# Optimization experiments

Hardware: AMD Instinct MI355X
Metric: run time of the kernel (lower is better)

The kernel has to match this reference:

```python
import jax, jax.numpy as jnp
import numpy as np

N = 100_000      # nodes
E = 1_600_000    # edges (avg degree 16)
D_IN, D_H, D_OUT = 128, 128, 64


def setup_inputs() -> dict:
    key = jax.random.key(0)
    ks = jax.random.split(key, 6)
    x = jax.random.normal(ks[0], (N, D_IN), jnp.float32)
    edge_index = jax.random.randint(ks[1], (2, E), 0, N, dtype=jnp.int32)
    W1 = jax.random.normal(ks[2], (D_IN, D_H), jnp.float32) / np.sqrt(D_IN)
    b1 = jnp.zeros((D_H,), jnp.float32)
    W2 = jax.random.normal(ks[3], (D_H, D_OUT), jnp.float32) / np.sqrt(D_H)
    b2 = jnp.zeros((D_OUT,), jnp.float32)
    return {"x": x, "edge_index": edge_index, "W1": W1, "b1": b1, "W2": W2, "b2": b2}


def _gcn_layer(x, W, b, src, dst, n_nodes):
    # PyG GCNConv: h = x @ W; symmetric norm with self-loops; scatter-add; + bias
    h = x @ W                                        # [N, D_out]
    deg = jax.ops.segment_sum(jnp.ones_like(dst, jnp.float32), dst,
                              num_segments=n_nodes)  # self-loops => deg >= 1
    dinv = jax.lax.rsqrt(deg)                        # deg^{-1/2}
    norm = dinv[src] * dinv[dst]                     # [E+N]
    msg = h[src] * norm[:, None]                     # gather + scale
    out = jax.ops.segment_sum(msg, dst, num_segments=n_nodes)  # scatter-add
    return out + b


def reference(x, edge_index, W1, b1, W2, b2):
    n = x.shape[0]
    loop = jnp.arange(n, dtype=edge_index.dtype)
    src = jnp.concatenate([edge_index[0], loop])     # add self-loops
    dst = jnp.concatenate([edge_index[1], loop])
    h = _gcn_layer(x, W1, b1, src, dst, n)
    h = jax.nn.relu(h)
    # dropout(p=0.5) is identity in eval mode
    out = _gcn_layer(h, W2, b2, src, dst, n)
    return out
```

## Files before the change

### kernel.cpp

```cpp
#include <hip/hip_runtime.h>
#include <hip/hip_bf16.h>


#define NTHREADS 256
#define BSH 9
#define NBMAX 256

typedef unsigned int uint;
typedef unsigned short ushort;
typedef __attribute__((ext_vector_type(8))) short short8;
typedef __attribute__((ext_vector_type(4))) float floatx4;

__device__ __forceinline__ uint pack_bf16(float a, float b) {
    __hip_bfloat162 h = __float22bfloat162_rn(make_float2(a, b));
    return *reinterpret_cast<uint*>(&h);
}
__device__ __forceinline__ float bf16_lo(uint q) { return __uint_as_float(q << 16); }
__device__ __forceinline__ float bf16_hi(uint q) { return __uint_as_float(q & 0xffff0000u); }

__global__ __launch_bounds__(256) void bucket_hist_kernel(
    const int* __restrict__ dst, int* __restrict__ bcnt, int e, int nb) {
    __shared__ int hist[NBMAX];
    int t = threadIdx.x;
    for (int b = t; b < nb; b += 256) hist[b] = 0;
    __syncthreads();
    int e0 = blockIdx.x * 2048;
#pragma unroll
    for (int v = 0; v < 2; v++) {
        int gi = e0 + t * 8 + v * 4;
        if (gi + 3 < e) {
            int4 d4 = *(const int4*)&dst[gi];
            atomicAdd(&hist[d4.x >> BSH], 1);
            atomicAdd(&hist[d4.y >> BSH], 1);
            atomicAdd(&hist[d4.z >> BSH], 1);
            atomicAdd(&hist[d4.w >> BSH], 1);
        } else {
            for (int j = 0; j < 4; j++)
                if (gi + j < e) atomicAdd(&hist[dst[gi + j] >> BSH], 1);
        }
    }
    __syncthreads();
    for (int b = t; b < nb; b += 256) {
        int v = hist[b];
        if (v) atomicAdd(&bcnt[b], v);
    }
}

__global__ void bucket_scan(const int* __restrict__ bcnt, int* __restrict__ bstart,
                            int* __restrict__ bcursor, int nb) {
    __shared__ int buf[NBMAX];
    int t = threadIdx.x;
    int v = (t < nb) ? bcnt[t] : 0;
    buf[t] = v;
    __syncthreads();
    int x = v;
    for (int off = 1; off < NBMAX; off <<= 1) {
        int y = (t >= off) ? buf[t - off] : 0;
        __syncthreads();
        x += y;
        buf[t] = x;
        __syncthreads();
    }
    if (t < nb) {
        bstart[t] = x - v;
        bcursor[t] = x - v;
    }
}

__global__ __launch_bounds__(256) void partition_kernel(
    const int* __restrict__ src, const int* __restrict__ dst,
    int* __restrict__ bcursor, int2* __restrict__ staged, int e, int nb) {
    __shared__ int eS[2048];
    __shared__ int eD[2048];
    __shared__ int hist[NBMAX];
    __shared__ int base[NBMAX];
    int t = threadIdx.x;
    int e0 = blockIdx.x * 2048;

    for (int b = t; b < nb; b += 256) hist[b] = 0;
    __syncthreads();
#pragma unroll
    for (int v = 0; v < 2; v++) {
        int li = t * 8 + v * 4;
        int gi = e0 + li;
        int4 s4, d4;
        if (gi + 3 < e) {
            s4 = *(const int4*)&src[gi];
            d4 = *(const int4*)&dst[gi];
        } else {
            const int* sp = &src[gi];
            const int* dp = &dst[gi];
            s4.x = (gi + 0 < e) ? sp[0] : 0;  d4.x = (gi + 0 < e) ? dp[0] : -1;
            s4.y = (gi + 1 < e) ? sp[1] : 0;  d4.y = (gi + 1 < e) ? dp[1] : -1;
            s4.z = (gi + 2 < e) ? sp[2] : 0;  d4.z = (gi + 2 < e) ? dp[2] : -1;
            s4.w = (gi + 3 < e) ? sp[3] : 0;  d4.w = (gi + 3 < e) ? dp[3] : -1;
        }
        *(int4*)&eS[li] = s4;
        *(int4*)&eD[li] = d4;
        if (d4.x >= 0) atomicAdd(&hist[d4.x >> BSH], 1);
        if (d4.y >= 0) atomicAdd(&hist[d4.y >> BSH], 1);
        if (d4.z >= 0) atomicAdd(&hist[d4.z >> BSH], 1);
        if (d4.w >= 0) atomicAdd(&hist[d4.w >> BSH], 1);
    }
    __syncthreads();
    for (int b = t; b < nb; b += 256) {
        int v = hist[b];
        base[b] = v ? atomicAdd(&bcursor[b], v) : 0;
        hist[b] = 0;
    }
    __syncthreads();
#pragma unroll
    for (int i = 0; i < 8; i++) {
        int li = t + i * 256;
        int d = eD[li];
        if (d >= 0) {
            int b = d >> BSH;
            int r = atomicAdd(&hist[b], 1);
            staged[base[b] + r] = make_int2(eS[li], d);
        }
    }
}

__global__ __launch_bounds__(256) void fine_csr_kernel(
    const int2* __restrict__ staged, const int* __restrict__ bstart,
    const int* __restrict__ bcnt, int4* __restrict__ meta,
    float* __restrict__ dinv, int* __restrict__ rec, int n) {
    __shared__ int lcnt[512];
    __shared__ int tsum[256];
    int b = blockIdx.x;
    int t = threadIdx.x;
    lcnt[t] = 0;
    lcnt[t + 256] = 0;
    __syncthreads();
    int s0 = bstart[b];
    int m = bcnt[b];
    for (int i = t; i < m; i += 256)
        atomicAdd(&lcnt[staged[s0 + i].y & 511], 1);
    __syncthreads();
    int v0 = lcnt[2 * t];
    int v1 = lcnt[2 * t + 1];
    int tot = v0 + v1;
    tsum[t] = tot;
    __syncthreads();
    int x = tot;
    for (int off = 1; off < 256; off <<= 1) {
        int y = (t >= off) ? tsum[t - off] : 0;
        __syncthreads();
        x += y;
        tsum[t] = x;
        __syncthreads();
    }
    int excl = x - tot;
    int node = (b << BSH) + 2 * t;
    if (node < n) {
        float di = rsqrtf((float)v0 + 1.0f);
        dinv[node] = di;
        meta[node] = make_int4(s0 + excl, v0, __float_as_int(di), __float_as_int(di * di));
    }
    if (node + 1 < n) {
        float di = rsqrtf((float)v1 + 1.0f);
        dinv[node + 1] = di;
        meta[node + 1] = make_int4(s0 + excl + v0, v1, __float_as_int(di), __float_as_int(di * di));
    }
    lcnt[2 * t] = s0 + excl;
    lcnt[2 * t + 1] = s0 + excl + v0;
    __syncthreads();
    for (int i = t; i < m; i += 256) {
        int2 ed = staged[s0 + i];
        int li = ed.y & 511;
        int pos = atomicAdd(&lcnt[li], 1);
        rec[pos] = ed.x;
    }
}

template <int COLS, bool XF32>
__global__ __launch_bounds__(256) void gemm_mfma(const void* __restrict__ Xv,
                                                 const float* __restrict__ W,
                                                 uint* __restrict__ Cq, int n) {
    __shared__ ushort sX[64 * 128];
    __shared__ ushort sWT[COLS * 128];
    int t = threadIdx.x;
    int rbase = blockIdx.x * 64;

    if (XF32) {
        const float* X = (const float*)Xv;
#pragma unroll
        for (int i = 0; i < 8; i++) {
            int f = t + 256 * i;
            int r = f >> 5;
            int c4 = f & 31;
            float4 v = make_float4(0.f, 0.f, 0.f, 0.f);
            int gr = rbase + r;
            if (gr < n) v = *(const float4*)(X + (size_t)gr * 128 + c4 * 4);
            uint lo = pack_bf16(v.x, v.y);
            uint hi = pack_bf16(v.z, v.w);
            int chunk = c4 >> 1;
            int sub = (c4 & 1) * 4;
            int off = r * 128 + (((chunk ^ (r & 15)) << 3) + sub);
            *(uint2*)&sX[off] = make_uint2(lo, hi);
        }
    } else {
        const ushort* X = (const ushort*)Xv;
#pragma unroll
        for (int i = 0; i < 4; i++) {
            int f = t + 256 * i;
            int r = f >> 4;
            int chunk = f & 15;
            uint4 v = make_uint4(0, 0, 0, 0);
            int gr = rbase + r;
            if (gr < n) v = *(const uint4*)(X + (size_t)gr * 128 + chunk * 8);
            int off = r * 128 + ((chunk ^ (r & 15)) << 3);
            *(uint4*)&sX[off] = v;
        }
    }
    {
        constexpr int UNITS = 64 * (COLS / 4);
        constexpr int PER_T = UNITS / 256;
#pragma unroll
        for (int i = 0; i < PER_T; i++) {
            int u = t + 256 * i;
            int kp = u / (COLS / 4);
            int n4 = u % (COLS / 4);
            int k = kp * 2;
            float4 w0 = *(const float4*)(W + (size_t)k * COLS + n4 * 4);
            float4 w1 = *(const float4*)(W + (size_t)(k + 1) * COLS + n4 * 4);
            int chunk = k >> 3;
            int sub = k & 7;
            const float* a0 = (const float*)&w0;
            const float* a1 = (const float*)&w1;
#pragma unroll
            for (int j = 0; j < 4; j++) {
                int nn = n4 * 4 + j;
                uint pk = pack_bf16(a0[j], a1[j]);
                int off = nn * 128 + (((chunk ^ (nn & 15)) << 3) + sub);
                *(uint*)&sWT[off] = pk;
            }
        }
    }
    __syncthreads();

    int lane = t & 63;
    int wave = t >> 6;
    int m = lane & 15;
    int q = lane >> 4;
    int r0 = wave * 16;

    floatx4 acc[COLS / 16];
#pragma unroll
    for (int c = 0; c < COLS / 16; c++) acc[c] = (floatx4){0.f, 0.f, 0.f, 0.f};

#pragma unroll
    for (int ks = 0; ks < 4; ks++) {
        int rr = r0 + m;
        int ca = (ks * 4 + q) ^ (rr & 15);
        short8 afrag = *(const short8*)&sX[rr * 128 + (ca << 3)];
#pragma unroll
        for (int c = 0; c < COLS / 16; c++) {
            int nn = c * 16 + m;
            int cb = (ks * 4 + q) ^ (nn & 15);
            short8 bfrag = *(const short8*)&sWT[nn * 128 + (cb << 3)];
            acc[c] = __builtin_amdgcn_mfma_f32_16x16x32_bf16(bfrag, afrag, acc[c], 0, 0, 0);
        }
    }

    int gr = rbase + r0 + m;
    if (gr < n) {
#pragma unroll
        for (int c = 0; c < COLS / 16; c++) {
            uint2 pk;
            pk.x = pack_bf16(acc[c][0], acc[c][1]);
            pk.y = pack_bf16(acc[c][2], acc[c][3]);
            *(uint2*)&Cq[(size_t)gr * (COLS / 2) + c * 8 + q * 2] = pk;
        }
    }
}

__global__ __launch_bounds__(512) void agg128_mm64(
    const uint* __restrict__ hq, const int* __restrict__ rec,
    const int4* __restrict__ meta, const float* __restrict__ dinv,
    const float* __restrict__ bias, const float* __restrict__ W2,
    uint* __restrict__ h2q, int n) {
    __shared__ ushort sWT[64 * 128];
    __shared__ ushort sg[16 * 128];
    int t = threadIdx.x;

#pragma unroll
    for (int i = 0; i < 2; i++) {
        int u = t + 512 * i;
        int kp = u >> 4;
        int n4 = u & 15;
        int k = kp * 2;
        float4 w0 = *(const float4*)(W2 + (size_t)k * 64 + n4 * 4);
        float4 w1 = *(const float4*)(W2 + (size_t)(k + 1) * 64 + n4 * 4);
        int chunk = k >> 3;
        int sub = k & 7;
        const float* a0f = (const float*)&w0;
        const float* a1f = (const float*)&w1;
#pragma unroll
        for (int j = 0; j < 4; j++) {
            int nn = n4 * 4 + j;
            uint pk = pack_bf16(a0f[j], a1f[j]);
            *(uint*)&sWT[nn * 128 + (((chunk ^ (nn & 15)) << 3) + sub)] = pk;
        }
    }

    int hw = t >> 5;
    int fl = t & 31;
    int nb0 = blockIdx.x * 16;
    int w = nb0 + hw;
    bool valid = w < n;
    int wsafe = valid ? w : 0;
    const uint2* h2 = (const uint2*)hq;

    int4 mt = meta[wsafe];
    int j0 = mt.x;
    int deg = valid ? mt.y : 0;
    float di = __int_as_float(mt.z);
    float swq = valid ? __int_as_float(mt.w) : 0.f;

    uint2 qs = h2[(size_t)wsafe * 32 + fl];
    float a0 = bf16_lo(qs.x) * swq, a1 = bf16_hi(qs.x) * swq;
    float a2 = bf16_lo(qs.y) * swq, a3 = bf16_hi(qs.y) * swq;

    const int* rp = rec + j0;
    int tt = 0;
    for (; tt + 8 <= deg; tt += 8) {
        uint2 q[8]; float wf[8];
#pragma unroll
        for (int u = 0; u < 8; u++) {
            int s = rp[tt + u];
            wf[u] = dinv[s] * di;
            q[u] = h2[(size_t)s * 32 + fl];
        }
#pragma unroll
        for (int u = 0; u < 8; u++) {
            a0 += bf16_lo(q[u].x) * wf[u]; a1 += bf16_hi(q[u].x) * wf[u];
            a2 += bf16_lo(q[u].y) * wf[u]; a3 += bf16_hi(q[u].y) * wf[u];
        }
    }
    for (; tt + 2 <= deg; tt += 2) {
        int s0i = rp[tt], s1i = rp[tt + 1];
        float w0v = dinv[s0i] * di, w1v = dinv[s1i] * di;
        uint2 q0 = h2[(size_t)s0i * 32 + fl];
        uint2 q1 = h2[(size_t)s1i * 32 + fl];
        a0 += bf16_lo(q0.x) * w0v + bf16_lo(q1.x) * w1v;
        a1 += bf16_hi(q0.x) * w0v + bf16_hi(q1.x) * w1v;
        a2 += bf16_lo(q0.y) * w0v + bf16_lo(q1.y) * w1v;
        a3 += bf16_hi(q0.y) * w0v + bf16_hi(q1.y) * w1v;
    }
    if (tt < deg) {
        int s = rp[tt];
        float wv = dinv[s] * di;
        uint2 q = h2[(size_t)s * 32 + fl];
        a0 += bf16_lo(q.x) * wv; a1 += bf16_hi(q.x) * wv;
        a2 += bf16_lo(q.y) * wv; a3 += bf16_hi(q.y) * wv;
    }

    float4 bb = *(const float4*)&bias[4 * fl];
    float o0 = fmaxf(a0 + bb.x, 0.f);
    float o1 = fmaxf(a1 + bb.y, 0.f);
    float o2 = fmaxf(a2 + bb.z, 0.f);
    float o3 = fmaxf(a3 + bb.w, 0.f);
    {
        int chunk = fl >> 1;
        int sub = (fl & 1) * 4;
        *(uint2*)&sg[hw * 128 + (((chunk ^ hw) << 3) + sub)] =
            make_uint2(pack_bf16(o0, o1), pack_bf16(o2, o3));
    }
    __syncthreads();

    int wave = t >> 6;
    int lane = t & 63;
    if (wave < 4) {
        int m = lane & 15;
        int q = lane >> 4;
        floatx4 acc = (floatx4){0.f, 0.f, 0.f, 0.f};
#pragma unroll
        for (int ks = 0; ks < 4; ks++) {
            int ca = (ks * 4 + q) ^ m;
            short8 afrag = *(const short8*)&sg[m * 128 + (ca << 3)];
            int nn = wave * 16 + m;
            int cb = (ks * 4 + q) ^ (nn & 15);
            short8 bfrag = *(const short8*)&sWT[nn * 128 + (cb << 3)];
            acc = __builtin_amdgcn_mfma_f32_16x16x32_bf16(bfrag, afrag, acc, 0, 0, 0);
        }
        int gr = nb0 + m;
        if (gr < n) {
            uint2 pk;
            pk.x = pack_bf16(acc[0], acc[1]);
            pk.y = pack_bf16(acc[2], acc[3]);
            *(uint2*)&h2q[(size_t)gr * 32 + wave * 8 + q * 2] = pk;
        }
    }
}

__global__ __launch_bounds__(256) void aggregate64q(
    const uint* __restrict__ hq, const int* __restrict__ rec,
    const int4* __restrict__ meta, const float* __restrict__ dinv,
    const float* __restrict__ bias, float* __restrict__ out, int n) {
    int w = (int)((blockIdx.x * blockDim.x + threadIdx.x) >> 5);
    if (w >= n) return;
    int fl = threadIdx.x & 31;

    int4 mt = meta[w];
    int j0 = mt.x;
    int deg = mt.y;
    float di = __int_as_float(mt.z);
    float swq = __int_as_float(mt.w);

    uint qs = hq[(size_t)w * 32 + fl];
    float a0 = bf16_lo(qs) * swq;
    float a1 = bf16_hi(qs) * swq;

    const int* rp = rec + j0;
    int t = 0;
    for (; t + 8 <= deg; t += 8) {
        uint q[8]; float wf[8];
#pragma unroll
        for (int u = 0; u < 8; u++) {
            int s = rp[t + u];
            wf[u] = dinv[s] * di;
            q[u] = hq[(size_t)s * 32 + fl];
        }
#pragma unroll
        for (int u = 0; u < 8; u++) {
            a0 += bf16_lo(q[u]) * wf[u];
            a1 += bf16_hi(q[u]) * wf[u];
        }
    }
    for (; t + 2 <= deg; t += 2) {
        int s0i = rp[t], s1i = rp[t + 1];
        float w0v = dinv[s0i] * di, w1v = dinv[s1i] * di;
        uint q0 = hq[(size_t)s0i * 32 + fl];
        uint q1 = hq[(size_t)s1i * 32 + fl];
        a0 += bf16_lo(q0) * w0v + bf16_lo(q1) * w1v;
        a1 += bf16_hi(q0) * w0v + bf16_hi(q1) * w1v;
    }
    if (t < deg) {
        int s = rp[t];
        float wv = dinv[s] * di;
        uint q = hq[(size_t)s * 32 + fl];
        a0 += bf16_lo(q) * wv;
        a1 += bf16_hi(q) * wv;
    }

    float2 bb = *(const float2*)&bias[2 * fl];
    float2 o;
    o.x = a0 + bb.x;
    o.y = a1 + bb.y;
    ((float2*)out)[(size_t)w * 32 + fl] = o;
}

extern "C" void kernel_launch(void* const* d_in, const int* in_sizes, int n_in,
                              void* d_out, int out_size, void* d_ws, size_t ws_size,
                              hipStream_t stream) {
    const float* x = (const float*)d_in[0];
    const int* edge = (const int*)d_in[1];
    const float* W1 = (const float*)d_in[2];
    const float* b1 = (const float*)d_in[3];
    const float* W2 = (const float*)d_in[4];
    const float* b2 = (const float*)d_in[5];

    const int N = in_sizes[0] / 128;
    const int E = in_sizes[1] / 2;
    const int* src = edge;
    const int* dst = edge + E;
    const int NB = (N + (1 << BSH) - 1) >> BSH;

    char* p = (char*)d_ws;
    int* bcnt = (int*)p;      p += NBMAX * 4;
    int* bstart = (int*)p;    p += NBMAX * 4;
    int* bcursor = (int*)p;   p += NBMAX * 4;
    float* dinv = (float*)p;  p += (size_t)N * 4;
    int4* meta = (int4*)p;    p += (size_t)N * 16;
    int* rec = (int*)p;       p += (size_t)E * 4;
    int2* staged = (int2*)p;  p += (size_t)E * 8;
    uint* hq = (uint*)p;      p += (size_t)N * 64 * 4;
    uint* h2q = (uint*)p;     p += (size_t)N * 32 * 4;

    float* out = (float*)d_out;
    const int eblocks = (E + 2047) / 2048;

    (void)hipMemsetAsync(bcnt, 0, NBMAX * 4, stream);
    bucket_hist_kernel<<<eblocks, 256, 0, stream>>>(dst, bcnt, E, NB);
    bucket_scan<<<1, NBMAX, 0, stream>>>(bcnt, bstart, bcursor, NB);
    partition_kernel<<<eblocks, 256, 0, stream>>>(src, dst, bcursor, staged, E, NB);
    fine_csr_kernel<<<NB, 256, 0, stream>>>(staged, bstart, bcnt, meta, dinv, rec, N);

    const int gblocks = (N + 63) / 64;

    gemm_mfma<128, true><<<gblocks, 256, 0, stream>>>(x, W1, hq, N);
    agg128_mm64<<<(N + 15) / 16, 512, 0, stream>>>(hq, rec, meta, dinv, b1, W2, h2q, N);
    aggregate64q<<<(N + 7) / 8, 256, 0, stream>>>(h2q, rec, meta, dinv, b2, out, N);
}
```

Measured before the change: 298.0 us.

## Fold source-side degree norm into GEMM epilogues and widen aggregation loads

Applies the source-side deg^-1/2 factor once per node in the GEMM and MM epilogues, so the aggregation loops no longer gather dinv per edge and only sum features before a final di scale. The aggregation kernels move from 32 lanes per node to 16 lanes per node (128-wide) and 8 lanes per node (64-wide) using 16-byte loads, and agg128_mm64 now handles 32 nodes per block with all 8 waves doing MFMA. This removes one dependent scattered load per edge and cuts instruction count, at the cost of rounding the pre-scaled values to bf16 and fewer lanes per node.

Measured after the change: 295.0 us. Within noise of the previous version (-1.0%).

```diff
diff --git a/kernel.cpp b/kernel.cpp
--- a/kernel.cpp
+++ b/kernel.cpp
@@ -176,7 +176,9 @@
 template <int COLS, bool XF32>
 __global__ __launch_bounds__(256) void gemm_mfma(const void* __restrict__ Xv,
                                                  const float* __restrict__ W,
-                                                 uint* __restrict__ Cq, int n) {
+                                                 uint* __restrict__ Cq,
+                                                 const float* __restrict__ dscale,
+                                                 int n) {
     __shared__ ushort sX[64 * 128];
     __shared__ ushort sWT[COLS * 128];
     int t = threadIdx.x;
@@ -265,11 +267,12 @@
 
     int gr = rbase + r0 + m;
     if (gr < n) {
+        float sc = dscale[gr];
 #pragma unroll
         for (int c = 0; c < COLS / 16; c++) {
             uint2 pk;
-            pk.x = pack_bf16(acc[c][0], acc[c][1]);
-            pk.y = pack_bf16(acc[c][2], acc[c][3]);
+            pk.x = pack_bf16(acc[c][0] * sc, acc[c][1] * sc);
+            pk.y = pack_bf16(acc[c][2] * sc, acc[c][3] * sc);
             *(uint2*)&Cq[(size_t)gr * (COLS / 2) + c * 8 + q * 2] = pk;
         }
     }
@@ -281,7 +284,7 @@
     const float* __restrict__ bias, const float* __restrict__ W2,
     uint* __restrict__ h2q, int n) {
     __shared__ ushort sWT[64 * 128];
-    __shared__ ushort sg[16 * 128];
+    __shared__ ushort sg[32 * 128];
     int t = threadIdx.x;
 
 #pragma unroll
@@ -304,151 +307,169 @@
         }
     }
 
-    int hw = t >> 5;
-    int fl = t & 31;
-    int nb0 = blockIdx.x * 16;
-    int w = nb0 + hw;
+    int qw = t >> 4;
+    int fl = t & 15;
+    int nb0 = blockIdx.x * 32;
+    int w = nb0 + qw;
     bool valid = w < n;
     int wsafe = valid ? w : 0;
-    const uint2* h2 = (const uint2*)hq;
+    const uint4* h4 = (const uint4*)hq;
 
     int4 mt = meta[wsafe];
     int j0 = mt.x;
     int deg = valid ? mt.y : 0;
     float di = __int_as_float(mt.z);
-    float swq = valid ? __int_as_float(mt.w) : 0.f;
-
-    uint2 qs = h2[(size_t)wsafe * 32 + fl];
-    float a0 = bf16_lo(qs.x) * swq, a1 = bf16_hi(qs.x) * swq;
-    float a2 = bf16_lo(qs.y) * swq, a3 = bf16_hi(qs.y) * swq;
+
+    uint4 qs = h4[(size_t)wsafe * 16 + fl];
+    float a0 = bf16_lo(qs.x), a1 = bf16_hi(qs.x);
+    float a2 = bf16_lo(qs.y), a3 = bf16_hi(qs.y);
+    float a4 = bf16_lo(qs.z), a5 = bf16_hi(qs.z);
+    float a6 = bf16_lo(qs.w), a7 = bf16_hi(qs.w);
+    if (!valid) { a0 = a1 = a2 = a3 = a4 = a5 = a6 = a7 = 0.f; }
 
     const int* rp = rec + j0;
     int tt = 0;
     for (; tt + 8 <= deg; tt += 8) {
-        uint2 q[8]; float wf[8];
+        int s[8]; uint4 q[8];
+#pragma unroll
+        for (int u = 0; u < 8; u++) s[u] = rp[tt + u];
+#pragma unroll
+        for (int u = 0; u < 8; u++) q[u] = h4[(size_t)s[u] * 16 + fl];
 #pragma unroll
         for (int u = 0; u < 8; u++) {
-            int s = rp[tt + u];
-            wf[u] = dinv[s] * di;
-            q[u] = h2[(size_t)s * 32 + fl];
-        }
-#pragma unroll
-        for (int u = 0; u < 8; u++) {
-            a0 += bf16_lo(q[u].x) * wf[u]; a1 += bf16_hi(q[u].x) * wf[u];
-            a2 += bf16_lo(q[u].y) * wf[u]; a3 += bf16_hi(q[u].y) * wf[u];
+            a0 += bf16_lo(q[u].x); a1 += bf16_hi(q[u].x);
+            a2 += bf16_lo(q[u].y); a3 += bf16_hi(q[u].y);
+            a4 += bf16_lo(q[u].z); a5 += bf16_hi(q[u].z);
+            a6 += bf16_lo(q[u].w); a7 += bf16_hi(q[u].w);
         }
     }
     for (; tt + 2 <= deg; tt += 2) {
         int s0i = rp[tt], s1i = rp[tt + 1];
-        float w0v = dinv[s0i] * di, w1v = dinv[s1i] * di;
-        uint2 q0 = h2[(size_t)s0i * 32 + fl];
-        uint2 q1 = h2[(size_t)s1i * 32 + fl];
-        a0 += bf16_lo(q0.x) * w0v + bf16_lo(q1.x) * w1v;
-        a1 += bf16_hi(q0.x) * w0v + bf16_hi(q1.x) * w1v;
-        a2 += bf16_lo(q0.y) * w0v + bf16_lo(q1.y) * w1v;
-        a3 += bf16_hi(q0.y) * w0v + bf16_hi(q1.y) * w1v;
+        uint4 q0 = h4[(size_t)s0i * 16 + fl];
+        uint4 q1 = h4[(size_t)s1i * 16 + fl];
+        a0 += bf16_lo(q0.x) + bf16_lo(q1.x);
+        a1 += bf16_hi(q0.x) + bf16_hi(q1.x);
+        a2 += bf16_lo(q0.y) + bf16_lo(q1.y);
+        a3 += bf16_hi(q0.y) + bf16_hi(q1.y);
+        a4 += bf16_lo(q0.z) + bf16_lo(q1.z);
+        a5 += bf16_hi(q0.z) + bf16_hi(q1.z);
+        a6 += bf16_lo(q0.w) + bf16_lo(q1.w);
+        a7 += bf16_hi(q0.w) + bf16_hi(q1.w);
     }
     if (tt < deg) {
         int s = rp[tt];
-        float wv = dinv[s] * di;
-        uint2 q = h2[(size_t)s * 32 + fl];
-        a0 += bf16_lo(q.x) * wv; a1 += bf16_hi(q.x) * wv;
-        a2 += bf16_lo(q.y) * wv; a3 += bf16_hi(q.y) * wv;
-    }
-
-    float4 bb = *(const float4*)&bias[4 * fl];
-    float o0 = fmaxf(a0 + bb.x, 0.f);
-    float o1 = fmaxf(a1 + bb.y, 0.f);
-    float o2 = fmaxf(a2 + bb.z, 0.f);
-    float o3 = fmaxf(a3 + bb.w, 0.f);
-    {
-        int chunk = fl >> 1;
-        int sub = (fl & 1) * 4;
-        *(uint2*)&sg[hw * 128 + (((chunk ^ hw) << 3) + sub)] =
-            make_uint2(pack_bf16(o0, o1), pack_bf16(o2, o3));
-    }
+        uint4 q0 = h4[(size_t)s * 16 + fl];
+        a0 += bf16_lo(q0.x); a1 += bf16_hi(q0.x);
+        a2 += bf16_lo(q0.y); a3 += bf16_hi(q0.y);
+        a4 += bf16_lo(q0.z); a5 += bf16_hi(q0.z);
+        a6 += bf16_lo(q0.w); a7 += bf16_hi(q0.w);
+    }
+
+    float4 bb0 = *(const float4*)&bias[8 * fl];
+    float4 bb1 = *(const float4*)&bias[8 * fl + 4];
+    uint4 pkv;
+    pkv.x = pack_bf16(fmaxf(di * a0 + bb0.x, 0.f), fmaxf(di * a1 + bb0.y, 0.f));
+    pkv.y = pack_bf16(fmaxf(di * a2 + bb0.z, 0.f), fmaxf(di * a3 + bb0.w, 0.f));
+    pkv.z = pack_bf16(fmaxf(di * a4 + bb1.x, 0.f), fmaxf(di * a5 + bb1.y, 0.f));
+    pkv.w = pack_bf16(fmaxf(di * a6 + bb1.z, 0.f), fmaxf(di * a7 + bb1.w, 0.f));
+    *(uint4*)&sg[qw * 128 + ((fl ^ (qw & 15)) << 3)] = pkv;
     __syncthreads();
 
     int wave = t >> 6;
     int lane = t & 63;
-    if (wave < 4) {
-        int m = lane & 15;
-        int q = lane >> 4;
-        floatx4 acc = (floatx4){0.f, 0.f, 0.f, 0.f};
-#pragma unroll
-        for (int ks = 0; ks < 4; ks++) {
-            int ca = (ks * 4 + q) ^ m;
-            short8 afrag = *(const short8*)&sg[m * 128 + (ca << 3)];
-            int nn = wave * 16 + m;
-            int cb = (ks * 4 + q) ^ (nn & 15);
-            short8 bfrag = *(const short8*)&sWT[nn * 128 + (cb << 3)];
-            acc = __builtin_amdgcn_mfma_f32_16x16x32_bf16(bfrag, afrag, acc, 0, 0, 0);
-        }
-        int gr = nb0 + m;
-        if (gr < n) {
-            uint2 pk;
-            pk.x = pack_bf16(acc[0], acc[1]);
-            pk.y = pack_bf16(acc[2], acc[3]);
-            *(uint2*)&h2q[(size_t)gr * 32 + wave * 8 + q * 2] = pk;
-        }
+    int m = lane & 15;
+    int qq = lane >> 4;
+    int rt = wave >> 2;
+    int ct = wave & 3;
+    floatx4 acc = (floatx4){0.f, 0.f, 0.f, 0.f};
+#pragma unroll
+    for (int ks = 0; ks < 4; ks++) {
+        int rr = rt * 16 + m;
+        int ca = (ks * 4 + qq) ^ (rr & 15);
+        short8 afrag = *(const short8*)&sg[rr * 128 + (ca << 3)];
+        int nn = ct * 16 + m;
+        int cb = (ks * 4 + qq) ^ (nn & 15);
+        short8 bfrag = *(const short8*)&sWT[nn * 128 + (cb << 3)];
+        acc = __builtin_amdgcn_mfma_f32_16x16x32_bf16(bfrag, afrag, acc, 0, 0, 0);
+    }
+    int gr = nb0 + rt * 16 + m;
+    if (gr < n) {
+        float sc = dinv[gr];
+        uint2 pk;
+        pk.x = pack_bf16(acc[0] * sc, acc[1] * sc);
+        pk.y = pack_bf16(acc[2] * sc, acc[3] * sc);
+        *(uint2*)&h2q[(size_t)gr * 32 + ct * 8 + qq * 2] = pk;
     }
 }
 
 __global__ __launch_bounds__(256) void aggregate64q(
     const uint* __restrict__ hq, const int* __restrict__ rec,
-    const int4* __restrict__ meta, const float* __restrict__ dinv,
-    const float* __restrict__ bias, float* __restrict__ out, int n) {
-    int w = (int)((blockIdx.x * blockDim.x + threadIdx.x) >> 5);
+    const int4* __restrict__ meta, const float* __restrict__ bias,
+    float* __restrict__ out, int n) {
+    int gt = blockIdx.x * 256 + threadIdx.x;
+    int w = gt >> 3;
     if (w >= n) return;
-    int fl = threadIdx.x & 31;
+    int fl = gt & 7;
 
     int4 mt = meta[w];
     int j0 = mt.x;
     int deg = mt.y;
     float di = __int_as_float(mt.z);
-    float swq = __int_as_float(mt.w);
-
-    uint qs = hq[(size_t)w * 32 + fl];
-    float a0 = bf16_lo(qs) * swq;
-    float a1 = bf16_hi(qs) * swq;
+    const uint4* h4 = (const uint4*)hq;
+
+    uint4 qs = h4[(size_t)w * 8 + fl];
+    float a0 = bf16_lo(qs.x), a1 = bf16_hi(qs.x);
+    float a2 = bf16_lo(qs.y), a3 = bf16_hi(qs.y);
+    float a4 = bf16_lo(qs.z), a5 = bf16_hi(qs.z);
+    float a6 = bf16_lo(qs.w), a7 = bf16_hi(qs.w);
 
     const int* rp = rec + j0;
-    int t = 0;
-    for (; t + 8 <= deg; t += 8) {
-        uint q[8]; float wf[8];
+    int tt = 0;
+    for (; tt + 8 <= deg; tt += 8) {
+        int s[8]; uint4 q[8];
+#pragma unroll
+        for (int u = 0; u < 8; u++) s[u] = rp[tt + u];
+#pragma unroll
+        for (int u = 0; u < 8; u++) q[u] = h4[(size_t)s[u] * 8 + fl];
 #pragma unroll
         for (int u = 0; u < 8; u++) {
-            int s = rp[t + u];
-            wf[u] = dinv[s] * di;
-            q[u] = hq[(size_t)s * 32 + fl];
-        }
-#pragma unroll
-        for (int u = 0; u < 8; u++) {
-            a0 += bf16_lo(q[u]) * wf[u];
-            a1 += bf16_hi(q[u]) * wf[u];
-        }
-    }
-    for (; t + 2 <= deg; t += 2) {
-        int s0i = rp[t], s1i = rp[t + 1];
-        float w0v = dinv[s0i] * di, w1v = dinv[s1i] * di;
-        uint q0 = hq[(size_t)s0i * 32 + fl];
-        uint q1 = hq[(size_t)s1i * 32 + fl];
-        a0 += bf16_lo(q0) * w0v + bf16_lo(q1) * w1v;
-        a1 += bf16_hi(q0) * w0v + bf16_hi(q1) * w1v;
-    }
-    if (t < deg) {
-        int s = rp[t];
-        float wv = dinv[s] * di;
-        uint q = hq[(size_t)s * 32 + fl];
-        a0 += bf16_lo(q) * wv;
-        a1 += bf16_hi(q) * wv;
-    }
-
-    float2 bb = *(const float2*)&bias[2 * fl];
-    float2 o;
-    o.x = a0 + bb.x;
-    o.y = a1 + bb.y;
-    ((float2*)out)[(size_t)w * 32 + fl] = o;
+            a0 += bf16_lo(q[u].x); a1 += bf16_hi(q[u].x);
+            a2 += bf16_lo(q[u].y); a3 += bf16_hi(q[u].y);
+            a4 += bf16_lo(q[u].z); a5 += bf16_hi(q[u].z);
+            a6 += bf16_lo(q[u].w); a7 += bf16_hi(q[u].w);
+        }
+    }
+    for (; tt + 2 <= deg; tt += 2) {
+        int s0i = rp[tt], s1i = rp[tt + 1];
+        uint4 q0 = h4[(size_t)s0i * 8 + fl];
+        uint4 q1 = h4[(size_t)s1i * 8 + fl];
+        a0 += bf16_lo(q0.x) + bf16_lo(q1.x);
+        a1 += bf16_hi(q0.x) + bf16_hi(q1.x);
+        a2 += bf16_lo(q0.y) + bf16_lo(q1.y);
+        a3 += bf16_hi(q0.y) + bf16_hi(q1.y);
+        a4 += bf16_lo(q0.z) + bf16_lo(q1.z);
+        a5 += bf16_hi(q0.z) + bf16_hi(q1.z);
+        a6 += bf16_lo(q0.w) + bf16_lo(q1.w);
+        a7 += bf16_hi(q0.w) + bf16_hi(q1.w);
+    }
+    if (tt < deg) {
+        int s = rp[tt];
+        uint4 q0 = h4[(size_t)s * 8 + fl];
+        a0 += bf16_lo(q0.x); a1 += bf16_hi(q0.x);
+        a2 += bf16_lo(q0.y); a3 += bf16_hi(q0.y);
+        a4 += bf16_lo(q0.z); a5 += bf16_hi(q0.z);
+        a6 += bf16_lo(q0.w); a7 += bf16_hi(q0.w);
+    }
+
+    float4 bb0 = *(const float4*)&bias[8 * fl];
+    float4 bb1 = *(const float4*)&bias[8 * fl + 4];
+    float4 o0, o1;
+    o0.x = di * a0 + bb0.x; o0.y = di * a1 + bb0.y;
+    o0.z = di * a2 + bb0.z; o0.w = di * a3 + bb0.w;
+    o1.x = di * a4 + bb1.x; o1.y = di * a5 + bb1.y;
+    o1.z = di * a6 + bb1.z; o1.w = di * a7 + bb1.w;
+    *(float4*)&out[(size_t)w * 64 + 8 * fl] = o0;
+    *(float4*)&out[(size_t)w * 64 + 8 * fl + 4] = o1;
 }
 
 extern "C" void kernel_launch(void* const* d_in, const int* in_sizes, int n_in,
@@ -489,7 +510,7 @@
 
     const int gblocks = (N + 63) / 64;
 
-    gemm_mfma<128, true><<<gblocks, 256, 0, stream>>>(x, W1, hq, N);
-    agg128_mm64<<<(N + 15) / 16, 512, 0, stream>>>(hq, rec, meta, dinv, b1, W2, h2q, N);
-    aggregate64q<<<(N + 7) / 8, 256, 0, stream>>>(h2q, rec, meta, dinv, b2, out, N);
-}
+    gemm_mfma<128, true><<<gblocks, 256, 0, stream>>>(x, W1, hq, dinv, N);
+    agg128_mm64<<<(N + 31) / 32, 512, 0, stream>>>(hq, rec, meta, dinv, b1, W2, h2q, N);
+    aggregate64q<<<(N * 8 + 255) / 256, 256, 0, stream>>>(h2q, rec, meta, b2, out, N);
+}
```
